# Kernel optimization log

Hardware: AMD Instinct MI355X
Metric: run time of the kernel (lower is better)

## Reference

```python
import jax, jax.numpy as jnp
import numpy as np

B, T, D, H = 4, 2048, 1152, 8
HD = D // H          # 144
ROT = HD             # full rotary
SCALE = HD ** -0.5


def _rotate_half(x):
    # x: [..., ROT]
    x1, x2 = x[..., : ROT // 2], x[..., ROT // 2 :]
    return jnp.concatenate([-x2, x1], axis=-1)


def _apply_rotary(q, k, cos, sin):
    # q,k: [B,H,T,HD]; cos,sin: [T,ROT] broadcast over B,H
    q_rot, q_pass = q[..., :ROT], q[..., ROT:]
    k_rot, k_pass = k[..., :ROT], k[..., ROT:]
    q = jnp.concatenate([q_rot * cos + _rotate_half(q_rot) * sin, q_pass], axis=-1)
    k = jnp.concatenate([k_rot * cos + _rotate_half(k_rot) * sin, k_pass], axis=-1)
    return q, k


def setup_inputs() -> dict:
    key = jax.random.key(0)
    ks = jax.random.split(key, 7)
    init = 1.0 / np.sqrt(D)  # keep activations well-scaled
    return {
        "x": jax.random.normal(ks[0], (B, T, D), dtype=jnp.float32),
        "cos": jax.random.uniform(ks[1], (T, ROT), dtype=jnp.float32),
        "sin": jax.random.uniform(ks[2], (T, ROT), dtype=jnp.float32),
        "Wq": jax.random.normal(ks[3], (D, D), dtype=jnp.float32) * init,
        "Wk": jax.random.normal(ks[4], (D, D), dtype=jnp.float32) * init,
        "Wv": jax.random.normal(ks[5], (D, D), dtype=jnp.float32) * init,
        "Wo": jax.random.normal(ks[6], (D, D), dtype=jnp.float32) * init,
    }


def reference(x, cos, sin, Wq, Wk, Wv, Wo):
    # nn.Linear(bias=False): y = x @ W.T
    def proj(W):
        y = jnp.einsum("btd,ed->bte", x, W)
        return y.reshape(B, T, H, HD).transpose(0, 2, 1, 3)  # [B,H,T,HD]

    q, k, v = proj(Wq), proj(Wk), proj(Wv)
    q, k = _apply_rotary(q, k, cos, sin)
    scores = jnp.einsum("bhqd,bhkd->bhqk", q, k) * SCALE
    attn = jax.nn.softmax(scores, axis=-1)
    o = jnp.einsum("bhqk,bhkd->bhqd", attn, v)
    o = o.transpose(0, 2, 1, 3).reshape(B, T, D)
    return jnp.einsum("btd,ed->bte", o, Wo)
```

## Files before the change

### kernel.cpp

```cpp
#include <hip/hip_runtime.h>
#include <cstdint>
#include <cstddef>

typedef __bf16 bf16;
typedef bf16 bf16x8 __attribute__((ext_vector_type(8)));
typedef bf16 bf16x4 __attribute__((ext_vector_type(4)));
typedef bf16 bf16x2 __attribute__((ext_vector_type(2)));
typedef float f32x4 __attribute__((ext_vector_type(4)));
typedef float f32x16 __attribute__((ext_vector_type(16)));
typedef uint32_t u32x2 __attribute__((ext_vector_type(2)));
typedef uint32_t u32x4 __attribute__((ext_vector_type(4)));

#define DEVI __device__ __forceinline__

#define CB 4
#define CT 2048
#define CD 1152
#define CH 8
#define CHD 144
#define CBT 8192

DEVI void gload_lds16(const void* g, void* l) {
  __builtin_amdgcn_global_load_lds(
      (const __attribute__((address_space(1))) void*)g,
      (__attribute__((address_space(3))) void*)l, 16, 0, 0);
}

DEVI f32x4 mfma16(bf16x8 a, bf16x8 b, f32x4 c) {
  return __builtin_amdgcn_mfma_f32_16x16x32_bf16(a, b, c, 0, 0, 0);
}
DEVI f32x16 mfma32(bf16x8 a, bf16x8 b, f32x16 c) {
  return __builtin_amdgcn_mfma_f32_32x32x16_bf16(a, b, c, 0, 0, 0);
}

DEVI uint32_t cvtpk(float lo, float hi) {
  uint32_t r;
  asm("v_cvt_pk_bf16_f32 %0, %1, %2" : "=v"(r) : "v"(lo), "v"(hi));
  return r;
}

DEVI f32x16 zero16() {
  f32x16 z;
#pragma unroll
  for (int i = 0; i < 16; ++i) z[i] = 0.f;
  return z;
}

__global__ __launch_bounds__(256) void k_cast(const float* __restrict__ in,
                                              bf16* __restrict__ out, int n8) {
  int i = blockIdx.x * 256 + threadIdx.x;
  if (i >= n8) return;
  const float4* p = (const float4*)in + (size_t)i * 2;
  float4 a = p[0], b = p[1];
  bf16x8 o;
  o[0] = (bf16)a.x; o[1] = (bf16)a.y; o[2] = (bf16)a.z; o[3] = (bf16)a.w;
  o[4] = (bf16)b.x; o[5] = (bf16)b.y; o[6] = (bf16)b.z; o[7] = (bf16)b.w;
  ((bf16x8*)out)[i] = o;
}

__global__ __launch_bounds__(256) void k_cast4(
    const float* __restrict__ a, const float* __restrict__ b,
    const float* __restrict__ c, const float* __restrict__ d,
    bf16* __restrict__ oa, bf16* __restrict__ ob,
    bf16* __restrict__ oc, bf16* __restrict__ od, int n8) {
  int w = blockIdx.y;
  const float* in = (w == 0) ? a : (w == 1) ? b : (w == 2) ? c : d;
  bf16* out = (w == 0) ? oa : (w == 1) ? ob : (w == 2) ? oc : od;
  int i = blockIdx.x * 256 + threadIdx.x;
  if (i >= n8) return;
  const float4* p = (const float4*)in + (size_t)i * 2;
  float4 x = p[0], y = p[1];
  bf16x8 o;
  o[0] = (bf16)x.x; o[1] = (bf16)x.y; o[2] = (bf16)x.z; o[3] = (bf16)x.w;
  o[4] = (bf16)y.x; o[5] = (bf16)y.y; o[6] = (bf16)y.z; o[7] = (bf16)y.w;
  ((bf16x8*)out)[i] = o;
}

template <bool BF16_OUT>
DEVI void gemm_body(const bf16* __restrict__ A, const bf16* __restrict__ W,
                    void* __restrict__ Cout, int M, int N, int K,
                    int bm0, int bn0) {
  constexpr int TBUF = 128 * 40;
  __shared__ __align__(16) bf16 As[2 * TBUF];
  __shared__ __align__(16) bf16 Bs[2 * TBUF];
  const int tid = threadIdx.x;
  const int lane = tid & 63, wid = tid >> 6;
  const int l15 = lane & 15, g = lane >> 4;
  const int wm = wid >> 1, wn = wid & 1;

  const bf16* asrc[3];
  const bf16* wsrc[3];
  int ldo[3];
  bool on[3];
#pragma unroll
  for (int c = 0; c < 3; ++c) {
    int li = tid + (c << 8);
    on[c] = (li < 640);
    int li2 = on[c] ? li : 0;
    int e0 = li2 << 3;
    int row = e0 / 40, col = e0 % 40;
    if (col >= 32) col = 24;
    asrc[c] = &A[(size_t)(bm0 + row) * K + col];
    wsrc[c] = &W[(size_t)(bn0 + row) * K + col];
    ldo[c] = (li2 & ~63) * 8;
  }

#define G_STAGE(k0, buf)                                                     \
  do {                                                                       \
    bf16* Ad = As + (buf)*TBUF;                                              \
    bf16* Bd = Bs + (buf)*TBUF;                                              \
    _Pragma("unroll") for (int c = 0; c < 3; ++c) if (on[c]) {               \
      gload_lds16(asrc[c] + (k0), Ad + ldo[c]);                              \
      gload_lds16(wsrc[c] + (k0), Bd + ldo[c]);                              \
    }                                                                        \
  } while (0)

  f32x4 acc[4][4];
  for (int mi = 0; mi < 4; ++mi)
    for (int ni = 0; ni < 4; ++ni) {
      acc[mi][ni][0] = 0.f; acc[mi][ni][1] = 0.f;
      acc[mi][ni][2] = 0.f; acc[mi][ni][3] = 0.f;
    }

  const int nk = K >> 5;
  G_STAGE(0, 0);
  __syncthreads();

  int cur = 0;
  for (int kt = 0; kt < nk; ++kt) {
    if (kt + 1 < nk) G_STAGE((kt + 1) << 5, cur ^ 1);
    __builtin_amdgcn_sched_barrier(0);

    const bf16* Ac = As + cur * TBUF;
    const bf16* Bc = Bs + cur * TBUF;
    bf16x8 af[4], bfr[4];
    for (int mi = 0; mi < 4; ++mi)
      af[mi] = *(const bf16x8*)&Ac[(wm * 64 + mi * 16 + l15) * 40 + g * 8];
    for (int ni = 0; ni < 4; ++ni)
      bfr[ni] = *(const bf16x8*)&Bc[(wn * 64 + ni * 16 + l15) * 40 + g * 8];
    __builtin_amdgcn_s_setprio(1);
    for (int mi = 0; mi < 4; ++mi)
      for (int ni = 0; ni < 4; ++ni)
        acc[mi][ni] = mfma16(af[mi], bfr[ni], acc[mi][ni]);
    __builtin_amdgcn_s_setprio(0);
    __syncthreads();
    cur ^= 1;
  }
#undef G_STAGE

  for (int mi = 0; mi < 4; ++mi)
    for (int ni = 0; ni < 4; ++ni)
      for (int r = 0; r < 4; ++r) {
        int rowg = bm0 + wm * 64 + mi * 16 + g * 4 + r;
        int colg = bn0 + wn * 64 + ni * 16 + l15;
        float v = acc[mi][ni][r];
        if (BF16_OUT)
          ((bf16*)Cout)[(size_t)rowg * N + colg] = (bf16)v;
        else
          ((float*)Cout)[(size_t)rowg * N + colg] = v;
      }
}

__global__ __launch_bounds__(256) void k_gemm_qkv(
    const bf16* __restrict__ A, const bf16* __restrict__ Wq,
    const bf16* __restrict__ Wk, const bf16* __restrict__ Wv,
    bf16* __restrict__ q, bf16* __restrict__ k, bf16* __restrict__ v) {
  const int nx = gridDim.x, ny = gridDim.y;
  const int nwg = nx * ny * gridDim.z;
  const int orig = (blockIdx.z * ny + blockIdx.y) * nx + blockIdx.x;
  const int logical = (orig & 7) * (nwg >> 3) + (orig >> 3);
  const int lx = logical % nx;
  const int rest = logical / nx;
  const int ly = rest % ny, lz = rest / ny;
  const bf16* W = (lz == 0) ? Wq : (lz == 1) ? Wk : Wv;
  bf16* out = (lz == 0) ? q : (lz == 1) ? k : v;
  gemm_body<true>(A, W, out, CBT, CD, CD, ly * 128, lx * 128);
}

__global__ __launch_bounds__(256) void k_gemm_out(
    const bf16* __restrict__ A, const bf16* __restrict__ W, float* __restrict__ out) {
  const int nx = gridDim.x, ny = gridDim.y;
  const int nwg = nx * ny;
  const int orig = blockIdx.y * nx + blockIdx.x;
  const int logical = (orig & 7) * (nwg >> 3) + (orig >> 3);
  const int lx = logical % nx, ly = logical / nx;
  gemm_body<false>(A, W, out, CBT, CD, CD, ly * 128, lx * 128);
}

__global__ __launch_bounds__(256) void k_rotary(bf16* __restrict__ q, bf16* __restrict__ k,
                                                const float* __restrict__ cosb,
                                                const float* __restrict__ sinb) {
  const int bt = blockIdx.x;
  const int t = bt & (CT - 1);
  const size_t rowoff = (size_t)bt * CD;
  const float* cr = cosb + (size_t)t * CHD;
  const float* sr = sinb + (size_t)t * CHD;
  for (int i = threadIdx.x; i < 288; i += 256) {
    int tensor = i / 144;
    int rem = i - tensor * 144;
    int h = rem / 18, jg = rem % 18;
    int j = jg * 4;
    float scl = tensor ? 1.0f : 0.120224587f;
    bf16* base = (tensor ? k : q) + rowoff + h * CHD;
    bf16x4 a = *(bf16x4*)&base[j];
    bf16x4 b2 = *(bf16x4*)&base[j + 72];
    f32x4 c1 = *(const f32x4*)&cr[j];
    f32x4 s1 = *(const f32x4*)&sr[j];
    f32x4 c2 = *(const f32x4*)&cr[j + 72];
    f32x4 s2 = *(const f32x4*)&sr[j + 72];
    bf16x4 o1, o2;
    for (int r = 0; r < 4; ++r) {
      float av = (float)a[r], bv = (float)b2[r];
      o1[r] = (bf16)((av * c1[r] - bv * s1[r]) * scl);
      o2[r] = (bf16)((bv * c2[r] + av * s2[r]) * scl);
    }
    *(bf16x4*)&base[j] = o1;
    *(bf16x4*)&base[j + 72] = o2;
  }
}

__global__ __launch_bounds__(256) void k_vtrans(const bf16* __restrict__ v, bf16* __restrict__ vT) {
  __shared__ bf16 tile[64][152];
  const int bh = blockIdx.y;
  const int b = bh >> 3, h = bh & 7;
  const int t0 = blockIdx.x * 64;
  for (int i8 = threadIdx.x; i8 < 64 * 18; i8 += 256) {
    int r = i8 / 18, c8 = i8 % 18;
    *(bf16x8*)&tile[r][c8 * 8] =
        *(const bf16x8*)&v[((size_t)(b * CT + t0 + r)) * CD + h * CHD + c8 * 8];
  }
  __syncthreads();
  for (int o = threadIdx.x; o < CHD * 64; o += 256) {
    int hd = o / 64, j = o & 63;
    vT[((size_t)(bh * CHD + hd)) * CT + t0 + j] = tile[j][hd];
  }
}

DEVI void build_pfrag(const f32x16& s, float m, float& ps, bf16x8& f0, bf16x8& f1) {
  uint32_t pk[8];
#pragma unroll
  for (int a = 0; a < 8; ++a) {
    float p0 = exp2f(s[2 * a] - m);
    float p1 = exp2f(s[2 * a + 1] - m);
    ps += p0 + p1;
    pk[a] = cvtpk(p0, p1);
  }
  u32x2 r02 = __builtin_amdgcn_permlane32_swap(pk[0], pk[2], false, false);
  u32x2 r13 = __builtin_amdgcn_permlane32_swap(pk[1], pk[3], false, false);
  u32x2 r46 = __builtin_amdgcn_permlane32_swap(pk[4], pk[6], false, false);
  u32x2 r57 = __builtin_amdgcn_permlane32_swap(pk[5], pk[7], false, false);
  u32x4 w0 = {r02[0], r13[0], r02[1], r13[1]};
  u32x4 w1 = {r46[0], r57[0], r46[1], r57[1]};
  f0 = __builtin_bit_cast(bf16x8, w0);
  f1 = __builtin_bit_cast(bf16x8, w1);
}

DEVI float max32(const f32x16& s0, const f32x16& s1) {
  float q0 = fmaxf(fmaxf(s0[0], s0[1]), fmaxf(s0[2], s0[3]));
  float q1 = fmaxf(fmaxf(s0[4], s0[5]), fmaxf(s0[6], s0[7]));
  float q2 = fmaxf(fmaxf(s0[8], s0[9]), fmaxf(s0[10], s0[11]));
  float q3 = fmaxf(fmaxf(s0[12], s0[13]), fmaxf(s0[14], s0[15]));
  float q4 = fmaxf(fmaxf(s1[0], s1[1]), fmaxf(s1[2], s1[3]));
  float q5 = fmaxf(fmaxf(s1[4], s1[5]), fmaxf(s1[6], s1[7]));
  float q6 = fmaxf(fmaxf(s1[8], s1[9]), fmaxf(s1[10], s1[11]));
  float q7 = fmaxf(fmaxf(s1[12], s1[13]), fmaxf(s1[14], s1[15]));
  return fmaxf(fmaxf(fmaxf(q0, q1), fmaxf(q2, q3)),
               fmaxf(fmaxf(q4, q5), fmaxf(q6, q7)));
}

__global__ __launch_bounds__(512, 2) void k_attn(const bf16* __restrict__ qg,
                                                 const bf16* __restrict__ kg,
                                                 const bf16* __restrict__ vT,
                                                 bf16* __restrict__ og) {
  const int lin = blockIdx.x;
  const int xcd = lin & 7, idx = lin >> 3;
  const int bh = ((idx & 3) << 3) | xcd;
  const int qx = idx >> 2;
  const int b = bh >> 3, h = bh & 7;
  const int q0 = qx << 8;
  const int tid = threadIdx.x, lane = tid & 63, wq = tid >> 6;
  const int l31 = lane & 31, hi = lane >> 5;
  const int hi16 = hi * 16;
  const int kxor = (l31 & 7) << 4;

  constexpr int KBUF = 64 * 192;
  constexpr int VBUF = 160 * 64;
  __shared__ __align__(16) bf16 Ks[2 * KBUF];
  __shared__ __align__(16) bf16 Vs[2 * VBUF];

  bf16x8 qf[9];
  {
    const bf16* qbase = qg + (size_t)(b * CT + q0 + wq * 32 + l31) * CD + h * CHD + hi * 8;
#pragma unroll
    for (int ks = 0; ks < 9; ++ks) qf[ks] = *(const bf16x8*)&qbase[ks * 16];
  }

  const bf16* ksrc[3];
  const bf16* vsrc[3];
  int kldo[3], vldo[3];
#pragma unroll
  for (int it = 0; it < 3; ++it) {
    int c = tid + it * 512;
    int krow = c / 24, kj = c - krow * 24;
    int kcol = (kj * 16) ^ ((krow & 7) << 4);
    if (kcol >= 288) kcol = 0;
    ksrc[it] = kg + (size_t)(b * CT + krow) * CD + h * CHD + (kcol >> 1);
    kldo[it] = ((tid & ~63) + it * 512) * 8;
    int vr = c >> 3, vj = c & 7;
    int vcol = (vj * 16) ^ ((vr & 7) << 4);
    if (vr > 143) vr = 143;
    vsrc[it] = vT + (size_t)(bh * CHD + vr) * CT + (vcol >> 1);
    vldo[it] = ((tid & ~63) + it * 512) * 8;
  }
  const bool vok2 = (tid < 128);

  if (tid < 256) {
    u32x4 z = {0u, 0u, 0u, 0u};
    int bsel = tid >> 7, off = tid & 127;
    *(u32x4*)(Vs + bsel * VBUF + 144 * 64 + off * 8) = z;
  }

#define STAGE_TILE(kv, buf)                                                 \
  do {                                                                      \
    bf16* Kn = Ks + (buf)*KBUF;                                             \
    bf16* Vn = Vs + (buf)*VBUF;                                             \
    _Pragma("unroll") for (int it = 0; it < 3; ++it)                        \
        gload_lds16(ksrc[it] + (size_t)(kv)*CD, Kn + kldo[it]);             \
    _Pragma("unroll") for (int it = 0; it < 2; ++it)                        \
        gload_lds16(vsrc[it] + (kv), Vn + vldo[it]);                        \
    if (vok2) gload_lds16(vsrc[2] + (kv), Vn + vldo[2]);                    \
  } while (0)

  STAGE_TILE(0, 0);
  __syncthreads();

  f32x16 oacc[5];
#pragma unroll
  for (int u = 0; u < 5; ++u) oacc[u] = zero16();
  float mrow = -__builtin_inff();
  float lsum = 0.f;

  int cur = 0;
  for (int t = 0; t < 32; ++t) {
    bf16* Kc = Ks + cur * KBUF;
    bf16* Vc = Vs + cur * VBUF;

    if (t < 31) STAGE_TILE((t + 1) << 6, cur ^ 1);
    __builtin_amdgcn_sched_barrier(0);

    const char* kr0 = (const char*)Kc + (size_t)l31 * 384;
    const char* kr1 = kr0 + 32 * 384;
    f32x16 s0 = zero16(), s1 = zero16();
    __builtin_amdgcn_s_setprio(1);
#pragma unroll
    for (int ks = 0; ks < 9; ++ks) {
      int off = (ks * 32 + hi16) ^ kxor;
      s0 = mfma32(*(const bf16x8*)(kr0 + off), qf[ks], s0);
      s1 = mfma32(*(const bf16x8*)(kr1 + off), qf[ks], s1);
    }
    __builtin_amdgcn_s_setprio(0);

    float mt = max32(s0, s1);
    mt = fmaxf(mt, __shfl_xor(mt, 32));

    if (mt > mrow + 8.0f) {
      float alpha = exp2f(mrow - mt);
      lsum *= alpha;
#pragma unroll
      for (int u = 0; u < 5; ++u) oacc[u] = oacc[u] * alpha;
      mrow = mt;
    }

    float ps = 0.f;
    bf16x8 pf0, pf1, pf2, pf3;
    build_pfrag(s0, mrow, ps, pf0, pf1);
    build_pfrag(s1, mrow, ps, pf2, pf3);
    ps += __shfl_xor(ps, 32);
    lsum += ps;

    __builtin_amdgcn_s_setprio(1);
#pragma unroll
    for (int u = 0; u < 5; ++u) {
      const char* vrow = (const char*)Vc + (size_t)(u * 32 + l31) * 128;
      oacc[u] = mfma32(*(const bf16x8*)(vrow + ((0 * 32 + hi16) ^ kxor)), pf0, oacc[u]);
      oacc[u] = mfma32(*(const bf16x8*)(vrow + ((1 * 32 + hi16) ^ kxor)), pf1, oacc[u]);
      oacc[u] = mfma32(*(const bf16x8*)(vrow + ((2 * 32 + hi16) ^ kxor)), pf2, oacc[u]);
      oacc[u] = mfma32(*(const bf16x8*)(vrow + ((3 * 32 + hi16) ^ kxor)), pf3, oacc[u]);
    }
    __builtin_amdgcn_s_setprio(0);

    __syncthreads();
    cur ^= 1;
  }
#undef STAGE_TILE

  float inv = 1.0f / lsum;
  bf16* ob = og + (size_t)(b * CT + q0 + wq * 32 + l31) * CD + h * CHD;
#pragma unroll
  for (int u = 0; u < 5; ++u) {
#pragma unroll
    for (int pr = 0; pr < 8; ++pr) {
      if (u == 4 && pr >= 4) continue;
      int hd = u * 32 + ((2 * pr) & 3) + 8 * (pr >> 1) + 4 * hi;
      bf16x2 w;
      w[0] = (bf16)(oacc[u][2 * pr] * inv);
      w[1] = (bf16)(oacc[u][2 * pr + 1] * inv);
      *(bf16x2*)&ob[hd] = w;
    }
  }
}

extern "C" void kernel_launch(void* const* d_in, const int* in_sizes, int n_in,
                              void* d_out, int out_size, void* d_ws, size_t ws_size,
                              hipStream_t stream) {
  const float* x = (const float*)d_in[0];
  const float* cosb = (const float*)d_in[1];
  const float* sinb = (const float*)d_in[2];
  const float* Wq = (const float*)d_in[3];
  const float* Wk = (const float*)d_in[4];
  const float* Wv = (const float*)d_in[5];
  const float* Wo = (const float*)d_in[6];

  char* ws = (char*)d_ws;
  bf16* xb   = (bf16*)(ws + 0);
  bf16* wqb  = (bf16*)(ws + 18874368);
  bf16* wkb  = (bf16*)(ws + 21528576);
  bf16* wvb  = (bf16*)(ws + 24182784);
  bf16* wob  = (bf16*)(ws + 26836992);
  bf16* qlin = (bf16*)(ws + 29491200);
  bf16* klin = (bf16*)(ws + 48365568);
  bf16* vlin = (bf16*)(ws + 67239936);
  bf16* vT   = (bf16*)(ws + 86114304);

  k_cast<<<4608, 256, 0, stream>>>(x, xb, CBT * CD / 8);
  k_cast4<<<dim3(648, 4), 256, 0, stream>>>(Wq, Wk, Wv, Wo, wqb, wkb, wvb, wob,
                                            CD * CD / 8);

  k_gemm_qkv<<<dim3(CD / 128, CBT / 128, 3), 256, 0, stream>>>(xb, wqb, wkb, wvb,
                                                               qlin, klin, vlin);
  k_rotary<<<CB * CT, 256, 0, stream>>>(qlin, klin, cosb, sinb);
  k_vtrans<<<dim3(CT / 64, CB * CH), 256, 0, stream>>>(vlin, vT);
  k_attn<<<256, 512, 0, stream>>>(qlin, klin, vT, xb);
  k_gemm_out<<<dim3(CD / 128, CBT / 128), 256, 0, stream>>>(xb, wob, (float*)d_out);
}
```

Measured before the change: 263.7 us.

## Halve attention block to 128 queries and shrink padded K tile stride

Measured after the change: 253.2 us. 1.04x faster.

```diff
diff --git a/kernel.cpp b/kernel.cpp
--- a/kernel.cpp
+++ b/kernel.cpp
@@ -268,7 +268,7 @@
                fmaxf(fmaxf(q4, q5), fmaxf(q6, q7)));
 }
 
-__global__ __launch_bounds__(512, 2) void k_attn(const bf16* __restrict__ qg,
+__global__ __launch_bounds__(256, 2) void k_attn(const bf16* __restrict__ qg,
                                                  const bf16* __restrict__ kg,
                                                  const bf16* __restrict__ vT,
                                                  bf16* __restrict__ og) {
@@ -277,13 +277,14 @@
   const int bh = ((idx & 3) << 3) | xcd;
   const int qx = idx >> 2;
   const int b = bh >> 3, h = bh & 7;
-  const int q0 = qx << 8;
+  const int q0 = qx << 7;
   const int tid = threadIdx.x, lane = tid & 63, wq = tid >> 6;
   const int l31 = lane & 31, hi = lane >> 5;
   const int hi16 = hi * 16;
-  const int kxor = (l31 & 7) << 4;
-
-  constexpr int KBUF = 64 * 192;
+  const int kx7 = l31 & 7;
+  const int kxor = kx7 << 4;
+
+  constexpr int KBUF = 64 * 144;
   constexpr int VBUF = 160 * 64;
   __shared__ __align__(16) bf16 Ks[2 * KBUF];
   __shared__ __align__(16) bf16 Vs[2 * VBUF];
@@ -295,26 +296,24 @@
     for (int ks = 0; ks < 9; ++ks) qf[ks] = *(const bf16x8*)&qbase[ks * 16];
   }
 
-  const bf16* ksrc[3];
-  const bf16* vsrc[3];
-  int kldo[3], vldo[3];
-#pragma unroll
-  for (int it = 0; it < 3; ++it) {
-    int c = tid + it * 512;
-    int krow = c / 24, kj = c - krow * 24;
-    int kcol = (kj * 16) ^ ((krow & 7) << 4);
-    if (kcol >= 288) kcol = 0;
-    ksrc[it] = kg + (size_t)(b * CT + krow) * CD + h * CHD + (kcol >> 1);
-    kldo[it] = ((tid & ~63) + it * 512) * 8;
+  const bf16* ksrc[5];
+  const bf16* vsrc[5];
+  int kldo[5], vldo[5];
+#pragma unroll
+  for (int it = 0; it < 5; ++it) {
+    int c = tid + it * 256;
+    if (c >= 1152) c = 0;
+    int krow = c / 18, kj = c - krow * 18;
+    int kgr = (kj < 16) ? (kj ^ (krow & 7)) : kj;
+    ksrc[it] = kg + (size_t)(b * CT + krow) * CD + h * CHD + kgr * 8;
+    kldo[it] = (c & ~63) * 8;
     int vr = c >> 3, vj = c & 7;
-    int vcol = (vj * 16) ^ ((vr & 7) << 4);
-    if (vr > 143) vr = 143;
-    vsrc[it] = vT + (size_t)(bh * CHD + vr) * CT + (vcol >> 1);
-    vldo[it] = ((tid & ~63) + it * 512) * 8;
-  }
-  const bool vok2 = (tid < 128);
-
-  if (tid < 256) {
+    int vgr = vj ^ (vr & 7);
+    vsrc[it] = vT + (size_t)(bh * CHD + vr) * CT + vgr * 8;
+    vldo[it] = (c & ~63) * 8;
+  }
+
+  {
     u32x4 z = {0u, 0u, 0u, 0u};
     int bsel = tid >> 7, off = tid & 127;
     *(u32x4*)(Vs + bsel * VBUF + 144 * 64 + off * 8) = z;
@@ -324,11 +323,14 @@
   do {                                                                      \
     bf16* Kn = Ks + (buf)*KBUF;                                             \
     bf16* Vn = Vs + (buf)*VBUF;                                             \
-    _Pragma("unroll") for (int it = 0; it < 3; ++it)                        \
-        gload_lds16(ksrc[it] + (size_t)(kv)*CD, Kn + kldo[it]);             \
-    _Pragma("unroll") for (int it = 0; it < 2; ++it)                        \
-        gload_lds16(vsrc[it] + (kv), Vn + vldo[it]);                        \
-    if (vok2) gload_lds16(vsrc[2] + (kv), Vn + vldo[2]);                    \
+    _Pragma("unroll") for (int it = 0; it < 4; ++it) {                      \
+      gload_lds16(ksrc[it] + (size_t)(kv)*CD, Kn + kldo[it]);               \
+      gload_lds16(vsrc[it] + (kv), Vn + vldo[it]);                          \
+    }                                                                       \
+    if (tid < 128) {                                                        \
+      gload_lds16(ksrc[4] + (size_t)(kv)*CD, Kn + kldo[4]);                 \
+      gload_lds16(vsrc[4] + (kv), Vn + vldo[4]);                            \
+    }                                                                       \
   } while (0)
 
   STAGE_TILE(0, 0);
@@ -348,13 +350,14 @@
     if (t < 31) STAGE_TILE((t + 1) << 6, cur ^ 1);
     __builtin_amdgcn_sched_barrier(0);
 
-    const char* kr0 = (const char*)Kc + (size_t)l31 * 384;
-    const char* kr1 = kr0 + 32 * 384;
+    const char* kr0 = (const char*)Kc + (size_t)l31 * 288;
+    const char* kr1 = kr0 + 32 * 288;
     f32x16 s0 = zero16(), s1 = zero16();
     __builtin_amdgcn_s_setprio(1);
 #pragma unroll
     for (int ks = 0; ks < 9; ++ks) {
-      int off = (ks * 32 + hi16) ^ kxor;
+      int cc = 2 * ks + hi;
+      int off = ((ks < 8) ? (cc ^ kx7) : cc) << 4;
       s0 = mfma32(*(const bf16x8*)(kr0 + off), qf[ks], s0);
       s1 = mfma32(*(const bf16x8*)(kr1 + off), qf[ks], s1);
     }
@@ -440,6 +443,6 @@
                                                                qlin, klin, vlin);
   k_rotary<<<CB * CT, 256, 0, stream>>>(qlin, klin, cosb, sinb);
   k_vtrans<<<dim3(CT / 64, CB * CH), 256, 0, stream>>>(vlin, vT);
-  k_attn<<<256, 512, 0, stream>>>(qlin, klin, vT, xb);
+  k_attn<<<512, 256, 0, stream>>>(qlin, klin, vT, xb);
   k_gemm_out<<<dim3(CD / 128, CBT / 128), 256, 0, stream>>>(xb, wob, (float*)d_out);
 }
```
